# Performance work log

Measured on AMD Instinct MI355X. Metric: run time of the kernel, lower is better.

Reference implementation:

```python
import jax, jax.numpy as jnp
import numpy as np

EPS = 1e-6
NH, HD = 8, 16            # num_heads, head_dim (dim=128)
KSS, DILS, HPR = (3, 5), (1, 2), (6, 2)  # kernel sizes, dilations, heads per range (favor_small)


def gelu(t):
    return jax.nn.gelu(t, approximate=False)


def conv1x1(x, w, b):
    # x: (B,C,H,W), w: (O,C), b: (O,)
    return jnp.einsum('oc,bchw->bohw', w, x) + b[None, :, None, None]


def dwconv(x, w, b, dil=1):
    # depthwise conv, w: (C,1,k,k)
    k = w.shape[-1]
    p = (k // 2) * dil
    y = jax.lax.conv_general_dilated(
        x, w, window_strides=(1, 1), padding=[(p, p), (p, p)],
        rhs_dilation=(dil, dil), feature_group_count=x.shape[1],
        dimension_numbers=('NCHW', 'OIHW', 'NCHW'))
    return y + b[None, :, None, None]


def ln2d(x, w, b):
    # LayerNorm over channel dim of NCHW
    mu = x.mean(axis=1, keepdims=True)
    var = ((x - mu) ** 2).mean(axis=1, keepdims=True)
    return (x - mu) * jax.lax.rsqrt(var + EPS) * w[None, :, None, None] + b[None, :, None, None]


def unfold(x, ks, dil):
    # x: (B,h,d,H,W) -> (B,h,d,L,H,W) with L=ks*ks neighborhood (row-major, matches F.unfold)
    B, h, d, H, W = x.shape
    p = (ks // 2) * dil
    xp = jnp.pad(x, ((0, 0), (0, 0), (0, 0), (p, p), (p, p)))
    patches = [xp[..., i * dil:i * dil + H, j * dil:j * dil + W]
               for i in range(ks) for j in range(ks)]
    return jnp.stack(patches, axis=3)


def neighborhood_attn(x, qkv_ws, qkv_bs, proj_w, proj_b):
    B, C, H, W = x.shape
    scale = HD ** -0.5
    outs, hs = [], 0
    for i in range(2):
        qkv = conv1x1(x, qkv_ws[i], qkv_bs[i]).reshape(B, 3, NH, HD, H, W)
        he = hs + HPR[i]
        q, k, v = qkv[:, 0, hs:he], qkv[:, 1, hs:he], qkv[:, 2, hs:he]
        k_nb = unfold(k, KSS[i], DILS[i])  # (B,h,d,L,H,W)
        v_nb = unfold(v, KSS[i], DILS[i])
        logits = jnp.einsum('bhdxy,bhdlxy->bhlxy', q * scale, k_nb)
        attn = jax.nn.softmax(logits, axis=2)
        outs.append(jnp.einsum('bhlxy,bhdlxy->bhdxy', attn, v_nb))
        hs = he
    out = jnp.concatenate(outs, axis=1).reshape(B, C, H, W)
    return conv1x1(out, proj_w, proj_b)


def msconvstar(x, fc1_w, fc1_b, dw_ws, dw_bs, fc2_w, fc2_b):
    h = conv1x1(x, fc1_w, fc1_b)                  # (B,192,H,W)
    xs = jnp.split(h, [64, 128], axis=1)          # channels [64,64,64] for dw_sizes (1,3,5)
    ys = [dwconv(t, w, b) for t, w, b in zip(xs, dw_ws, dw_bs)]
    h = h + jnp.concatenate(ys, axis=1)
    x1, x2 = jnp.split(h, 2, axis=1)
    return conv1x1(gelu(x1) * x2, fc2_w, fc2_b)


def cascaded_sparse(x, dw0_w, dw0_b, dw1_w, dw1_b, pw_w, pw_b):
    x = gelu(dwconv(x, dw0_w, dw0_b, dil=1))
    x = gelu(dwconv(x, dw1_w, dw1_b, dil=2))
    return conv1x1(x, pw_w, pw_b)


def setup_inputs() -> dict:
    key = jax.random.key(0)
    ks = jax.random.split(key, 24)
    C, HID = 128, 192

    def p(k, shape, s=0.02):
        return jax.random.normal(k, shape, jnp.float32) * s

    d = {'x': jax.random.normal(ks[0], (4, C, 80, 80), jnp.float32)}
    for i in (1, 2, 3, 4):
        d[f'n{i}_w'] = jnp.ones((C,), jnp.float32)
        d[f'n{i}_b'] = jnp.zeros((C,), jnp.float32)
    d['qkv0_w'] = p(ks[1], (3 * C, C)); d['qkv0_b'] = jnp.zeros((3 * C,), jnp.float32)
    d['qkv1_w'] = p(ks[2], (3 * C, C)); d['qkv1_b'] = jnp.zeros((3 * C,), jnp.float32)
    d['ma_proj_w'] = p(ks[3], (C, C)); d['ma_proj_b'] = jnp.zeros((C,), jnp.float32)
    for pre, k0 in (('m1', 4), ('m2', 10)):
        d[f'{pre}_fc1_w'] = p(ks[k0], (HID, C)); d[f'{pre}_fc1_b'] = jnp.zeros((HID,), jnp.float32)
        for j, dk in enumerate((1, 3, 5)):
            d[f'{pre}_dw{j}_w'] = p(ks[k0 + 1 + j], (64, 1, dk, dk))
            d[f'{pre}_dw{j}_b'] = jnp.zeros((64,), jnp.float32)
        d[f'{pre}_fc2_w'] = p(ks[k0 + 4], (C, HID // 2)); d[f'{pre}_fc2_b'] = jnp.zeros((C,), jnp.float32)
    d['sma_dw0_w'] = p(ks[16], (C, 1, 3, 3)); d['sma_dw0_b'] = jnp.zeros((C,), jnp.float32)
    d['sma_dw1_w'] = p(ks[17], (C, 1, 3, 3)); d['sma_dw1_b'] = jnp.zeros((C,), jnp.float32)
    d['sma_pw_w'] = p(ks[18], (C, C)); d['sma_pw_b'] = jnp.zeros((C,), jnp.float32)
    return d


def reference(x, n1_w, n1_b, n2_w, n2_b, n3_w, n3_b, n4_w, n4_b,
              qkv0_w, qkv0_b, qkv1_w, qkv1_b, ma_proj_w, ma_proj_b,
              m1_fc1_w, m1_fc1_b, m1_dw0_w, m1_dw0_b, m1_dw1_w, m1_dw1_b,
              m1_dw2_w, m1_dw2_b, m1_fc2_w, m1_fc2_b,
              sma_dw0_w, sma_dw0_b, sma_dw1_w, sma_dw1_b, sma_pw_w, sma_pw_b,
              m2_fc1_w, m2_fc1_b, m2_dw0_w, m2_dw0_b, m2_dw1_w, m2_dw1_b,
              m2_dw2_w, m2_dw2_b, m2_fc2_w, m2_fc2_b):
    x = x + neighborhood_attn(ln2d(x, n1_w, n1_b), (qkv0_w, qkv1_w), (qkv0_b, qkv1_b), ma_proj_w, ma_proj_b)
    x = x + msconvstar(ln2d(x, n2_w, n2_b), m1_fc1_w, m1_fc1_b,
                       (m1_dw0_w, m1_dw1_w, m1_dw2_w), (m1_dw0_b, m1_dw1_b, m1_dw2_b), m1_fc2_w, m1_fc2_b)
    x = x + cascaded_sparse(ln2d(x, n3_w, n3_b), sma_dw0_w, sma_dw0_b, sma_dw1_w, sma_dw1_b, sma_pw_w, sma_pw_b)
    x = x + msconvstar(ln2d(x, n4_w, n4_b), m2_fc1_w, m2_fc1_b,
                       (m2_dw0_w, m2_dw1_w, m2_dw2_w), (m2_dw0_b, m2_dw1_b, m2_dw2_b), m2_fc2_w, m2_fc2_b)
    return x
```

## Files before the change

### kernel.cpp

```cpp
#include <hip/hip_runtime.h>
#include <math.h>

#define Hn 80
#define Wn 80
#define HWn 6400

typedef unsigned short u16;
typedef __attribute__((ext_vector_type(8))) short s16x8;
typedef __attribute__((ext_vector_type(4))) float f32x4;

__device__ __forceinline__ float gelu_exact(float v) {
  return 0.5f * v * (1.f + erff(v * 0.70710678118654752f));
}
__device__ __forceinline__ u16 f2bf(float x) {
  unsigned u = __float_as_uint(x);
  return (u16)((u + 0x7fffu + ((u >> 16) & 1u)) >> 16);
}
__device__ __forceinline__ float bf2f(u16 h) {
  return __uint_as_float(((unsigned)h) << 16);
}
typedef __attribute__((address_space(1))) const unsigned int* gptr_t;
typedef __attribute__((address_space(3))) unsigned int* lptr_t;
__device__ __forceinline__ void gld16(const void* g, void* l) {
  __builtin_amdgcn_global_load_lds((gptr_t)g, (lptr_t)l, 16, 0, 0);
}
__device__ __forceinline__ void ld16h(const u16* p, float* f) {
  uint4 a = *(const uint4*)p;
  uint4 c = *(const uint4*)(p + 8);
  unsigned w[8] = {a.x, a.y, a.z, a.w, c.x, c.y, c.z, c.w};
  #pragma unroll
  for (int j = 0; j < 8; ++j) {
    f[2 * j]     = __uint_as_float(w[j] << 16);
    f[2 * j + 1] = __uint_as_float(w[j] & 0xffff0000u);
  }
}

__global__ __launch_bounds__(256) void wprep_k(
    const float* __restrict__ q0w, const float* __restrict__ q0b,
    const float* __restrict__ q1w, const float* __restrict__ q1b,
    const float* __restrict__ projw, const float* __restrict__ f1w_1,
    const float* __restrict__ f2w_1, const float* __restrict__ pww,
    const float* __restrict__ f1w_2, const float* __restrict__ f2w_2,
    u16* Wq, float* Bq, u16* Wp, u16* Wf1a, u16* Wf2a, u16* Wpw, u16* Wf1b, u16* Wf2b) {
  int idx = blockIdx.x * 256 + threadIdx.x;
  if (idx < 49152) {
    int r = idx >> 7, ic = idx & 127;
    int sel = r >> 7, c = r & 127;
    const float* src = ((c >> 4) < 6 ? q0w : q1w);
    Wq[idx] = f2bf(src[(size_t)(sel * 128 + c) * 128 + ic]);
    return;
  }
  idx -= 49152;
  if (idx < 16384) { Wp[idx] = f2bf(projw[idx]); return; }
  idx -= 16384;
  if (idx < 24576) { Wf1a[idx] = f2bf(f1w_1[idx]); return; }
  idx -= 24576;
  if (idx < 16384) { int oc = idx >> 7, ic = idx & 127;
    Wf2a[idx] = ic < 96 ? f2bf(f2w_1[oc * 96 + ic]) : (u16)0; return; }
  idx -= 16384;
  if (idx < 16384) { Wpw[idx] = f2bf(pww[idx]); return; }
  idx -= 16384;
  if (idx < 24576) { Wf1b[idx] = f2bf(f1w_2[idx]); return; }
  idx -= 24576;
  if (idx < 16384) { int oc = idx >> 7, ic = idx & 127;
    Wf2b[idx] = ic < 96 ? f2bf(f2w_2[oc * 96 + ic]) : (u16)0; return; }
  idx -= 16384;
  if (idx < 384) {
    int sel = idx >> 7, c = idx & 127;
    Bq[idx] = ((c >> 4) < 6 ? q0b : q1b)[sel * 128 + c];
  }
}

__global__ __launch_bounds__(256) void ln_k(const float* __restrict__ in,
    const float* __restrict__ gw, const float* __restrict__ gb, u16* __restrict__ outv) {
  __shared__ float sS[4][64];
  __shared__ float sQ[4][64];
  __shared__ unsigned sT[64 * 64];
  const int b = blockIdx.y;
  const int p0 = blockIdx.x * 64;
  const int tid = threadIdx.x;
  const int px = tid & 63;
  const int cg = tid >> 6;
  const float* ip = in + (size_t)b * 128 * HWn + p0 + px;
  float s = 0.f, q = 0.f;
  #pragma unroll 8
  for (int c = cg * 32; c < cg * 32 + 32; ++c) { float v = ip[(size_t)c * HWn]; s += v; q += v * v; }
  sS[cg][px] = s; sQ[cg][px] = q;
  __syncthreads();
  float S = sS[0][px] + sS[1][px] + sS[2][px] + sS[3][px];
  float Q = sQ[0][px] + sQ[1][px] + sQ[2][px] + sQ[3][px];
  float mu = S * (1.f / 128.f);
  float rs = rsqrtf(Q * (1.f / 128.f) - mu * mu + 1e-6f);
  #pragma unroll
  for (int j = 0; j < 16; ++j) {
    int c0 = cg * 32 + 2 * j;
    float v0 = ip[(size_t)c0 * HWn];
    float v1 = ip[(size_t)(c0 + 1) * HWn];
    v0 = (v0 - mu) * rs * gw[c0] + gb[c0];
    v1 = (v1 - mu) * rs * gw[c0 + 1] + gb[c0 + 1];
    int wc = cg * 16 + j;
    sT[px * 64 + (wc ^ (px & 31))] = (unsigned)f2bf(v0) | ((unsigned)f2bf(v1) << 16);
  }
  __syncthreads();
  u16* ob = outv + ((size_t)b * HWn + p0) * 128;
  #pragma unroll
  for (int it = 0; it < 4; ++it) {
    int opx = it * 16 + (tid >> 4);
    int chunk = tid & 15;
    unsigned w[4];
    #pragma unroll
    for (int j = 0; j < 4; ++j)
      w[j] = sT[opx * 64 + ((chunk * 4 + j) ^ (opx & 31))];
    *(uint4*)(ob + (size_t)opx * 128 + chunk * 8) = make_uint4(w[0], w[1], w[2], w[3]);
  }
}

__device__ __forceinline__ s16x8 ldfrag(const u16* s, int row, int gk) {
  return *(const s16x8*)(s + row * 128 + ((gk ^ (row & 7)) << 3));
}

template<int ORIENT, int SPLITQ, int H16>
__global__ __launch_bounds__(256) void gemm_k(
    const u16* __restrict__ Xg, const u16* __restrict__ Wg,
    const float* __restrict__ bias, u16* __restrict__ outH, int OCT) {
  __shared__ u16 sX[128 * 128];
  __shared__ u16 sW[64 * 128];
  const int tid = threadIdx.x, lane = tid & 63, wv = tid >> 6;
  const int b = blockIdx.y;
  const int px0 = blockIdx.x * 128;
  const int oc0 = blockIdx.z * 64;
  const u16* xb = Xg + ((size_t)b * HWn + px0) * 128;
  const u16* wb = Wg + (size_t)oc0 * 128;
  #pragma unroll
  for (int i = 0; i < 8; ++i) {
    int o16 = (wv * 8 + i) * 64 + lane;
    int r = o16 >> 4, g = o16 & 15;
    gld16(xb + (size_t)r * 128 + ((g ^ (r & 7)) << 3), (char*)sX + (size_t)(wv * 8 + i) * 1024);
  }
  #pragma unroll
  for (int i = 0; i < 4; ++i) {
    int o16 = (wv * 4 + i) * 64 + lane;
    int r = o16 >> 4, g = o16 & 15;
    gld16(wb + (size_t)r * 128 + ((g ^ (r & 7)) << 3), (char*)sW + (size_t)(wv * 4 + i) * 1024);
  }
  __syncthreads();
  const int l15 = lane & 15, l4 = lane >> 4;
  if (ORIENT == 0) {
    f32x4 acc[4][2] = {};
    #pragma unroll
    for (int ks = 0; ks < 4; ++ks) {
      int gk = ks * 4 + l4;
      s16x8 a[4], bb[2];
      #pragma unroll
      for (int mi = 0; mi < 4; ++mi) a[mi] = ldfrag(sW, mi * 16 + l15, gk);
      #pragma unroll
      for (int ni = 0; ni < 2; ++ni) bb[ni] = ldfrag(sX, wv * 32 + ni * 16 + l15, gk);
      #pragma unroll
      for (int mi = 0; mi < 4; ++mi)
        #pragma unroll
        for (int ni = 0; ni < 2; ++ni)
          acc[mi][ni] = __builtin_amdgcn_mfma_f32_16x16x32_bf16(a[mi], bb[ni], acc[mi][ni], 0, 0, 0);
    }
    #pragma unroll
    for (int mi = 0; mi < 4; ++mi) {
      #pragma unroll
      for (int rr = 0; rr < 4; ++rr) {
        int oc = oc0 + mi * 16 + l4 * 4 + rr;
        float bv = bias[oc];
        #pragma unroll
        for (int ni = 0; ni < 2; ++ni) {
          size_t idx = ((size_t)b * OCT + oc) * HWn + px0 + wv * 32 + ni * 16 + l15;
          outH[idx] = f2bf(acc[mi][ni][rr] + bv);
        }
      }
    }
  } else {
    f32x4 acc[2][4] = {};
    #pragma unroll
    for (int ks = 0; ks < 4; ++ks) {
      int gk = ks * 4 + l4;
      s16x8 a[2], bb[4];
      #pragma unroll
      for (int mi = 0; mi < 2; ++mi) a[mi] = ldfrag(sX, wv * 32 + mi * 16 + l15, gk);
      #pragma unroll
      for (int ni = 0; ni < 4; ++ni) bb[ni] = ldfrag(sW, ni * 16 + l15, gk);
      #pragma unroll
      for (int mi = 0; mi < 2; ++mi)
        #pragma unroll
        for (int ni = 0; ni < 4; ++ni)
          acc[mi][ni] = __builtin_amdgcn_mfma_f32_16x16x32_bf16(a[mi], bb[ni], acc[mi][ni], 0, 0, 0);
    }
    #pragma unroll
    for (int ni = 0; ni < 4; ++ni) {
      int oc = oc0 + ni * 16 + l15;
      float bv = bias[oc];
      #pragma unroll
      for (int mi = 0; mi < 2; ++mi) {
        #pragma unroll
        for (int rr = 0; rr < 4; ++rr) {
          int px = px0 + wv * 32 + mi * 16 + l4 * 4 + rr;
          float v = acc[mi][ni][rr] + bv;
          u16 hv = f2bf(v);
          int sel = oc >> 7, c = oc & 127;
          int head = c >> 4, d = c & 15;
          outH[((((size_t)sel * 8 + head) * 4 + b) * HWn + px) * 16 + d] = hv;
        }
      }
    }
  }
}

template<int EPI>
__global__ __launch_bounds__(256) void gemm64_k(
    const u16* __restrict__ Xg, const u16* __restrict__ Wg,
    const float* __restrict__ bias, const float* __restrict__ resid,
    float* __restrict__ outF, u16* __restrict__ outLN, float2* __restrict__ stats,
    const float* __restrict__ gw, const float* __restrict__ gb) {
  __shared__ u16 sX[64 * 128];
  __shared__ u16 sW[128 * 128];
  const int tid = threadIdx.x, lane = tid & 63, wv = tid >> 6;
  const int b = blockIdx.y;
  const int px0 = blockIdx.x * 64;
  const u16* xb = Xg + ((size_t)b * HWn + px0) * 128;
  #pragma unroll
  for (int i = 0; i < 4; ++i) {
    int o16 = (wv * 4 + i) * 64 + lane;
    int r = o16 >> 4, g = o16 & 15;
    gld16(xb + (size_t)r * 128 + ((g ^ (r & 7)) << 3), (char*)sX + (size_t)(wv * 4 + i) * 1024);
  }
  #pragma unroll
  for (int i = 0; i < 8; ++i) {
    int o16 = (wv * 8 + i) * 64 + lane;
    int r = o16 >> 4, g = o16 & 15;
    gld16(Wg + (size_t)r * 128 + ((g ^ (r & 7)) << 3), (char*)sW + (size_t)(wv * 8 + i) * 1024);
  }
  __syncthreads();
  const int l15 = lane & 15, l4 = lane >> 4;
  f32x4 acc[8] = {};
  #pragma unroll
  for (int ks = 0; ks < 4; ++ks) {
    int gk = ks * 4 + l4;
    s16x8 bb = ldfrag(sX, wv * 16 + l15, gk);
    #pragma unroll
    for (int mi = 0; mi < 8; ++mi) {
      s16x8 a = ldfrag(sW, mi * 16 + l15, gk);
      acc[mi] = __builtin_amdgcn_mfma_f32_16x16x32_bf16(a, bb, acc[mi], 0, 0, 0);
    }
  }
  const int pxg = px0 + wv * 16 + l15;
  float v[8][4];
  float s = 0.f, q = 0.f;
  #pragma unroll
  for (int mi = 0; mi < 8; ++mi) {
    #pragma unroll
    for (int rr = 0; rr < 4; ++rr) {
      int oc = mi * 16 + l4 * 4 + rr;
      float t = acc[mi][rr] + bias[oc];
      t += resid[((size_t)b * 128 + oc) * HWn + pxg];
      v[mi][rr] = t;
      s += t;
      q = fmaf(t, t, q);
    }
  }
  #pragma unroll
  for (int mi = 0; mi < 8; ++mi)
    #pragma unroll
    for (int rr = 0; rr < 4; ++rr) {
      int oc = mi * 16 + l4 * 4 + rr;
      outF[((size_t)b * 128 + oc) * HWn + pxg] = v[mi][rr];
    }
  if (EPI == 0) return;
  s += __shfl_xor(s, 16); s += __shfl_xor(s, 32);
  q += __shfl_xor(q, 16); q += __shfl_xor(q, 32);
  float mu = s * (1.f / 128.f);
  float rs = rsqrtf(q * (1.f / 128.f) - mu * mu + 1e-6f);
  if (EPI == 1) {
    u16* lp = outLN + ((size_t)b * HWn + pxg) * 128;
    #pragma unroll
    for (int mi = 0; mi < 8; ++mi) {
      int oc0 = mi * 16 + l4 * 4;
      unsigned lo = (unsigned)f2bf((v[mi][0] - mu) * rs * gw[oc0] + gb[oc0])
                  | ((unsigned)f2bf((v[mi][1] - mu) * rs * gw[oc0 + 1] + gb[oc0 + 1]) << 16);
      unsigned hi = (unsigned)f2bf((v[mi][2] - mu) * rs * gw[oc0 + 2] + gb[oc0 + 2])
                  | ((unsigned)f2bf((v[mi][3] - mu) * rs * gw[oc0 + 3] + gb[oc0 + 3]) << 16);
      *(uint2*)(lp + oc0) = make_uint2(lo, hi);
    }
  } else {
    if (l4 == 0) stats[(size_t)b * HWn + pxg] = make_float2(mu, rs);
  }
}

template<int KS, int DIL>
__device__ __forceinline__ void natt_body(const u16* __restrict__ qkv,
    u16* __restrict__ out, u16* __restrict__ sK, u16* __restrict__ sV,
    int b, int h, int ty0, int tx0, int tid, int ly, int lx) {
  constexpr int HALO = DIL * (KS / 2);
  constexpr int D = 16 + 2 * HALO;
  const u16* Qb = qkv + (((size_t)h * 4 + b) * HWn) * 16;
  const u16* Kb = qkv + ((((size_t)8 + h) * 4 + b) * HWn) * 16;
  const u16* Vb = qkv + ((((size_t)16 + h) * 4 + b) * HWn) * 16;
  for (int i = tid; i < D * D * 2; i += 256) {
    int pxi = i >> 1, half = i & 1;
    int ey = pxi / D, ex = pxi - ey * D;
    int gy = ty0 - HALO + ey, gx = tx0 - HALO + ex;
    uint4 kv = make_uint4(0, 0, 0, 0), vv = make_uint4(0, 0, 0, 0);
    if (gy >= 0 && gy < Hn && gx >= 0 && gx < Wn) {
      size_t off = (size_t)(gy * Wn + gx) * 16 + half * 8;
      kv = *(const uint4*)(Kb + off);
      vv = *(const uint4*)(Vb + off);
    }
    *(uint4*)(sK + pxi * 16 + half * 8) = kv;
    *(uint4*)(sV + pxi * 16 + half * 8) = vv;
  }
  const int p = (ty0 + ly) * Wn + tx0 + lx;
  float qv[16];
  ld16h(Qb + (size_t)p * 16, qv);
  #pragma unroll
  for (int d = 0; d < 16; ++d) qv[d] *= 0.25f;
  __syncthreads();
  constexpr int L = KS * KS;
  float lg[L];
  #pragma unroll
  for (int i = 0; i < KS; ++i) {
    #pragma unroll
    for (int j = 0; j < KS; ++j) {
      float kvv[16];
      ld16h(sK + (size_t)((ly + i * DIL) * D + lx + j * DIL) * 16, kvv);
      float a = 0.f;
      #pragma unroll
      for (int d = 0; d < 16; ++d) a = fmaf(qv[d], kvv[d], a);
      lg[i * KS + j] = a;
    }
  }
  float mx = lg[0];
  #pragma unroll
  for (int l = 1; l < L; ++l) mx = fmaxf(mx, lg[l]);
  float sum = 0.f;
  #pragma unroll
  for (int l = 0; l < L; ++l) { float e = __expf(lg[l] - mx); lg[l] = e; sum += e; }
  float inv = 1.f / sum;
  float acc[16];
  #pragma unroll
  for (int d = 0; d < 16; ++d) acc[d] = 0.f;
  #pragma unroll
  for (int i = 0; i < KS; ++i) {
    #pragma unroll
    for (int j = 0; j < KS; ++j) {
      float vv[16];
      ld16h(sV + (size_t)((ly + i * DIL) * D + lx + j * DIL) * 16, vv);
      float wl = lg[i * KS + j] * inv;
      #pragma unroll
      for (int d = 0; d < 16; ++d) acc[d] = fmaf(wl, vv[d], acc[d]);
    }
  }
  unsigned wst[8];
  #pragma unroll
  for (int j = 0; j < 8; ++j)
    wst[j] = (unsigned)f2bf(acc[2 * j]) | ((unsigned)f2bf(acc[2 * j + 1]) << 16);
  u16* op = out + ((size_t)b * HWn + p) * 128 + h * 16;
  *(uint4*)op = make_uint4(wst[0], wst[1], wst[2], wst[3]);
  *(uint4*)(op + 8) = make_uint4(wst[4], wst[5], wst[6], wst[7]);
}

__global__ __launch_bounds__(256) void natt_k(const u16* __restrict__ qkv,
                                              u16* __restrict__ out) {
  __shared__ u16 sK[24 * 24 * 16];
  __shared__ u16 sV[24 * 24 * 16];
  const int b = blockIdx.y, h = blockIdx.z;
  const int tile = blockIdx.x;
  const int ty0 = (tile / 5) * 16, tx0 = (tile % 5) * 16;
  const int tid = threadIdx.x;
  const int ly = tid >> 4, lx = tid & 15;
  if (h < 6) natt_body<3, 1>(qkv, out, sK, sV, b, h, ty0, tx0, tid, ly, lx);
  else       natt_body<5, 2>(qkv, out, sK, sV, b, h, ty0, tx0, tid, ly, lx);
}

template<int R>
__device__ __forceinline__ void stage_plane(const u16* __restrict__ plane,
                                            float* __restrict__ s,
                                            int ty0, int tx0, int tid) {
  constexpr int D = 16 + 2 * R, PD = D + 1;
  #pragma unroll
  for (int i = tid; i < D * D; i += 256) {
    int ey = i / D, ex = i - ey * D;
    int gy = ty0 - R + ey, gx = tx0 - R + ex;
    float v = 0.f;
    if (gy >= 0 && gy < Hn && gx >= 0 && gx < Wn) v = bf2f(plane[gy * Wn + gx]);
    s[ey * PD + ex] = v;
  }
}

template<int R>
__device__ __forceinline__ float dw_from_lds(const float* __restrict__ s, int ly, int lx,
                                             const float* __restrict__ w, float bv) {
  constexpr int PD = 16 + 2 * R + 1;
  float center = s[(ly + R) * PD + (lx + R)];
  float acc = bv;
  #pragma unroll
  for (int i = 0; i < 2 * R + 1; ++i)
    #pragma unroll
    for (int j = 0; j < 2 * R + 1; ++j)
      acc = fmaf(w[i * (2 * R + 1) + j], s[(ly + i) * PD + (lx + j)], acc);
  return center + acc;
}

template<int R1, int R2>
__device__ __forceinline__ void star_pairs(const u16* __restrict__ hb,
    const float* __restrict__ w0, const float* __restrict__ b0,
    const float* __restrict__ w1, const float* __restrict__ b1,
    const float* __restrict__ w2, const float* __restrict__ b2,
    float* __restrict__ s1_0, float* __restrict__ s1_1,
    float* __restrict__ s2_0, float* __restrict__ s2_1,
    int z, int ty0, int tx0, int tid, int ly, int lx, unsigned* __restrict__ res) {
  if (R1 > 0) stage_plane<R1>(hb + (size_t)(z * 8) * HWn, s1_0, ty0, tx0, tid);
  stage_plane<R2>(hb + (size_t)(z * 8 + 96) * HWn, s2_0, ty0, tx0, tid);
  __syncthreads();
  #pragma unroll 1
  for (int pi = 0; pi < 8; ++pi) {
    int c1 = z * 8 + pi;
    int c2 = c1 + 96;
    float* s1c = (pi & 1) ? s1_1 : s1_0;
    float* s2c = (pi & 1) ? s2_1 : s2_0;
    if (pi < 7) {
      float* s1n = (pi & 1) ? s1_0 : s1_1;
      float* s2n = (pi & 1) ? s2_0 : s2_1;
      if (R1 > 0) stage_plane<R1>(hb + (size_t)(c1 + 1) * HWn, s1n, ty0, tx0, tid);
      stage_plane<R2>(hb + (size_t)(c2 + 1) * HWn, s2n, ty0, tx0, tid);
    }
    float h1;
    if constexpr (R1 == 0) {
      float cen = bf2f(hb[(size_t)c1 * HWn + (ty0 + ly) * Wn + tx0 + lx]);
      h1 = cen + fmaf(cen, w0[c1], b0[c1]);
    } else {
      h1 = dw_from_lds<R1>(s1c, ly, lx, w1 + (c1 - 64) * 9, b1[c1 - 64]);
    }
    float h2;
    if constexpr (R2 == 1) {
      h2 = dw_from_lds<1>(s2c, ly, lx, w1 + (c2 - 64) * 9, b1[c2 - 64]);
    } else {
      h2 = dw_from_lds<2>(s2c, ly, lx, w2 + (c2 - 128) * 25, b2[c2 - 128]);
    }
    u16 gv = f2bf(gelu_exact(h1) * h2);
    if (pi & 1) res[pi >> 1] |= ((unsigned)gv) << 16;
    else        res[pi >> 1] = (unsigned)gv;
    __syncthreads();
  }
}

__global__ __launch_bounds__(256) void star_k(const u16* __restrict__ hbuf,
    const float* __restrict__ w0, const float* __restrict__ b0,
    const float* __restrict__ w1, const float* __restrict__ b1,
    const float* __restrict__ w2, const float* __restrict__ b2,
    u16* __restrict__ g) {
  __shared__ float s1_0[18 * 19];
  __shared__ float s1_1[18 * 19];
  __shared__ float s2_0[20 * 21];
  __shared__ float s2_1[20 * 21];
  const int b = blockIdx.y, z = blockIdx.z;
  const int tile = blockIdx.x;
  const int ty0 = (tile / 5) * 16, tx0 = (tile % 5) * 16;
  const int tid = threadIdx.x;
  const int ly = tid >> 4, lx = tid & 15;
  const u16* hb = hbuf + (size_t)b * 192 * HWn;
  unsigned res[4];
  if (z < 4)      star_pairs<0, 1>(hb, w0, b0, w1, b1, w2, b2, s1_0, s1_1, s2_0, s2_1, z, ty0, tx0, tid, ly, lx, res);
  else if (z < 8) star_pairs<0, 2>(hb, w0, b0, w1, b1, w2, b2, s1_0, s1_1, s2_0, s2_1, z, ty0, tx0, tid, ly, lx, res);
  else            star_pairs<1, 2>(hb, w0, b0, w1, b1, w2, b2, s1_0, s1_1, s2_0, s2_1, z, ty0, tx0, tid, ly, lx, res);
  const int px = (ty0 + ly) * Wn + tx0 + lx;
  *(uint4*)(g + ((size_t)b * HWn + px) * 128 + z * 8) = make_uint4(res[0], res[1], res[2], res[3]);
  if (z < 4)
    *(uint4*)(g + ((size_t)b * HWn + px) * 128 + 96 + z * 8) = make_uint4(0, 0, 0, 0);
}

__global__ __launch_bounds__(256) void dwgf_k(const float* __restrict__ xin,
    const float2* __restrict__ st,
    const float* __restrict__ gw, const float* __restrict__ gb,
    const float* __restrict__ w1, const float* __restrict__ b1,
    const float* __restrict__ w2, const float* __restrict__ b2,
    u16* __restrict__ out) {
  __shared__ float sA[22 * 23];
  __shared__ float sB[20 * 21];
  __shared__ float sMu[22 * 22];
  __shared__ float sRs[22 * 22];
  const int b = blockIdx.y, z = blockIdx.z;
  const int tile = blockIdx.x;
  const int ty0 = (tile / 5) * 16, tx0 = (tile % 5) * 16;
  const int tid = threadIdx.x;
  const int ly = tid >> 4, lx = tid & 15;
  #pragma unroll
  for (int i = tid; i < 22 * 22; i += 256) {
    int ey = i / 22, ex = i - ey * 22;
    int gy = ty0 - 3 + ey, gx = tx0 - 3 + ex;
    float2 s = make_float2(0.f, 0.f);
    if (gy >= 0 && gy < Hn && gx >= 0 && gx < Wn) s = st[(size_t)b * HWn + gy * Wn + gx];
    sMu[i] = s.x; sRs[i] = s.y;
  }
  const float* xb = xin + (size_t)b * 128 * HWn;
  unsigned res[4];
  #pragma unroll 1
  for (int ci = 0; ci < 8; ++ci) {
    int c = z * 8 + ci;
    const float* xp = xb + (size_t)c * HWn;
    float gwc = gw[c], gbc = gb[c];
    __syncthreads();
    #pragma unroll
    for (int i = tid; i < 22 * 22; i += 256) {
      int ey = i / 22, ex = i - ey * 22;
      int gy = ty0 - 3 + ey, gx = tx0 - 3 + ex;
      float v = 0.f;
      if (gy >= 0 && gy < Hn && gx >= 0 && gx < Wn)
        v = (xp[gy * Wn + gx] - sMu[i]) * sRs[i] * gwc + gbc;
      sA[ey * 23 + ex] = v;
    }
    __syncthreads();
    #pragma unroll
    for (int j = tid; j < 20 * 20; j += 256) {
      int by = j / 20, bx = j - by * 20;
      int gy = ty0 - 2 + by, gx = tx0 - 2 + bx;
      float r = 0.f;
      if (gy >= 0 && gy < Hn && gx >= 0 && gx < Wn) {
        float acc = b1[c];
        #pragma unroll
        for (int di = 0; di < 3; ++di)
          #pragma unroll
          for (int dj = 0; dj < 3; ++dj)
            acc = fmaf(w1[c * 9 + di * 3 + dj], sA[(by + di) * 23 + (bx + dj)], acc);
        r = gelu_exact(acc);
      }
      sB[by * 21 + bx] = r;
    }
    __syncthreads();
    float acc = b2[c];
    #pragma unroll
    for (int di = 0; di < 3; ++di)
      #pragma unroll
      for (int dj = 0; dj < 3; ++dj)
        acc = fmaf(w2[c * 9 + di * 3 + dj], sB[(ly + 2 * di) * 21 + (lx + 2 * dj)], acc);
    float r = gelu_exact(acc);
    u16 gv = f2bf(r);
    if (ci & 1) res[ci >> 1] |= ((unsigned)gv) << 16;
    else        res[ci >> 1] = (unsigned)gv;
  }
  const int px = (ty0 + ly) * Wn + tx0 + lx;
  *(uint4*)(out + ((size_t)b * HWn + px) * 128 + z * 8) = make_uint4(res[0], res[1], res[2], res[3]);
}

extern "C" void kernel_launch(void* const* d_in, const int* in_sizes, int n_in,
                              void* d_out, int out_size, void* d_ws, size_t ws_size,
                              hipStream_t stream) {
  (void)in_sizes; (void)n_in; (void)out_size; (void)ws_size;
  const float* x      = (const float*)d_in[0];
  const float* n1w    = (const float*)d_in[1];
  const float* n1b    = (const float*)d_in[2];
  const float* n2w    = (const float*)d_in[3];
  const float* n2b    = (const float*)d_in[4];
  const float* n3w    = (const float*)d_in[5];
  const float* n3b    = (const float*)d_in[6];
  const float* n4w    = (const float*)d_in[7];
  const float* n4b    = (const float*)d_in[8];
  const float* qkv0w  = (const float*)d_in[9];
  const float* qkv0b  = (const float*)d_in[10];
  const float* qkv1w  = (const float*)d_in[11];
  const float* qkv1b  = (const float*)d_in[12];
  const float* projw  = (const float*)d_in[13];
  const float* projb  = (const float*)d_in[14];
  const float* m1fc1w = (const float*)d_in[15];
  const float* m1fc1b = (const float*)d_in[16];
  const float* m1dw0w = (const float*)d_in[17];
  const float* m1dw0b = (const float*)d_in[18];
  const float* m1dw1w = (const float*)d_in[19];
  const float* m1dw1b = (const float*)d_in[20];
  const float* m1dw2w = (const float*)d_in[21];
  const float* m1dw2b = (const float*)d_in[22];
  const float* m1fc2w = (const float*)d_in[23];
  const float* m1fc2b = (const float*)d_in[24];
  const float* smadw0w = (const float*)d_in[25];
  const float* smadw0b = (const float*)d_in[26];
  const float* smadw1w = (const float*)d_in[27];
  const float* smadw1b = (const float*)d_in[28];
  const float* smapww  = (const float*)d_in[29];
  const float* smapwb  = (const float*)d_in[30];
  const float* m2fc1w = (const float*)d_in[31];
  const float* m2fc1b = (const float*)d_in[32];
  const float* m2dw0w = (const float*)d_in[33];
  const float* m2dw0b = (const float*)d_in[34];
  const float* m2dw1w = (const float*)d_in[35];
  const float* m2dw1b = (const float*)d_in[36];
  const float* m2dw2w = (const float*)d_in[37];
  const float* m2dw2b = (const float*)d_in[38];
  const float* m2fc2w = (const float*)d_in[39];
  const float* m2fc2b = (const float*)d_in[40];

  float* out = (float*)d_out;
  char* wsb = (char*)d_ws;
  u16*  QKV = (u16*)(wsb + 0);
  u16*  Hb16 = (u16*)(wsb + 0);
  u16*  LNo = (u16*)(wsb + 19660800);
  u16*  ATT = (u16*)(wsb + 26214400);
  u16*  T2  = (u16*)(wsb + 32768000);
  char* wp = wsb + 39321600;
  u16* Wq    = (u16*)wp;  wp += 98304;
  u16* Wproj = (u16*)wp;  wp += 32768;
  u16* Wf1a  = (u16*)wp;  wp += 49152;
  u16* Wf2a  = (u16*)wp;  wp += 32768;
  u16* Wpw   = (u16*)wp;  wp += 32768;
  u16* Wf1b  = (u16*)wp;  wp += 49152;
  u16* Wf2b  = (u16*)wp;  wp += 32768;
  float* Bq  = (float*)wp; wp += 2048;
  float2* Stats = (float2*)wp;

  dim3 blk(256);
  wprep_k<<<642, blk, 0, stream>>>(qkv0w, qkv0b, qkv1w, qkv1b, projw, m1fc1w, m1fc2w,
                                   smapww, m2fc1w, m2fc2w,
                                   Wq, Bq, Wproj, Wf1a, Wf2a, Wpw, Wf1b, Wf2b);

  ln_k<<<dim3(100, 4), blk, 0, stream>>>(x, n1w, n1b, LNo);
  gemm_k<1, 1, 0><<<dim3(50, 4, 6), blk, 0, stream>>>(LNo, Wq, Bq, QKV, 384);
  natt_k<<<dim3(25, 4, 8), blk, 0, stream>>>(QKV, ATT);
  gemm64_k<1><<<dim3(100, 4), blk, 0, stream>>>(ATT, Wproj, projb, x, out, LNo, nullptr, n2w, n2b);

  gemm_k<0, 0, 1><<<dim3(50, 4, 3), blk, 0, stream>>>(LNo, Wf1a, m1fc1b, Hb16, 192);
  star_k<<<dim3(25, 4, 12), blk, 0, stream>>>(Hb16, m1dw0w, m1dw0b, m1dw1w, m1dw1b, m1dw2w, m1dw2b, ATT);
  gemm64_k<2><<<dim3(100, 4), blk, 0, stream>>>(ATT, Wf2a, m1fc2b, out, out, nullptr, Stats, nullptr, nullptr);

  dwgf_k<<<dim3(25, 4, 16), blk, 0, stream>>>(out, Stats, n3w, n3b,
                                              smadw0w, smadw0b, smadw1w, smadw1b, T2);
  gemm64_k<1><<<dim3(100, 4), blk, 0, stream>>>(T2, Wpw, smapwb, out, out, LNo, nullptr, n4w, n4b);

  gemm_k<0, 0, 1><<<dim3(50, 4, 3), blk, 0, stream>>>(LNo, Wf1b, m2fc1b, Hb16, 192);
  star_k<<<dim3(25, 4, 12), blk, 0, stream>>>(Hb16, m2dw0w, m2dw0b, m2dw1w, m2dw1b, m2dw2w, m2dw2b, ATT);
  gemm64_k<0><<<dim3(100, 4), blk, 0, stream>>>(ATT, Wf2b, m2fc2b, out, out, nullptr, nullptr, nullptr, nullptr);
}
```

Before: 166.3 us.

## Halve gemm64 pixel tile with cross-wave LN reduction; use polynomial erf in GELU

```diff
diff --git a/kernel.cpp b/kernel.cpp
--- a/kernel.cpp
+++ b/kernel.cpp
@@ -10,7 +10,13 @@
 typedef __attribute__((ext_vector_type(4))) float f32x4;
 
 __device__ __forceinline__ float gelu_exact(float v) {
-  return 0.5f * v * (1.f + erff(v * 0.70710678118654752f));
+  float x = fabsf(v) * 0.70710678118654752f;
+  float t = 1.f / (1.f + 0.3275911f * x);
+  float p = t * (0.254829592f + t * (-0.284496736f + t * (1.421413741f +
+            t * (-1.453152027f + t * 1.061405429f))));
+  float erfa = 1.f - p * __expf(-x * x);
+  float erfv = copysignf(erfa, v);
+  return 0.5f * v * (1.f + erfv);
 }
 __device__ __forceinline__ u16 f2bf(float x) {
   unsigned u = __float_as_uint(x);
@@ -216,69 +222,73 @@
     const float* __restrict__ bias, const float* __restrict__ resid,
     float* __restrict__ outF, u16* __restrict__ outLN, float2* __restrict__ stats,
     const float* __restrict__ gw, const float* __restrict__ gb) {
-  __shared__ u16 sX[64 * 128];
+  __shared__ u16 sX[32 * 128];
   __shared__ u16 sW[128 * 128];
   const int tid = threadIdx.x, lane = tid & 63, wv = tid >> 6;
   const int b = blockIdx.y;
-  const int px0 = blockIdx.x * 64;
+  const int px0 = blockIdx.x * 32;
   const u16* xb = Xg + ((size_t)b * HWn + px0) * 128;
   #pragma unroll
-  for (int i = 0; i < 4; ++i) {
-    int o16 = (wv * 4 + i) * 64 + lane;
+  for (int i = 0; i < 2; ++i) {
+    int o16 = i * 256 + tid;
     int r = o16 >> 4, g = o16 & 15;
-    gld16(xb + (size_t)r * 128 + ((g ^ (r & 7)) << 3), (char*)sX + (size_t)(wv * 4 + i) * 1024);
+    gld16(xb + (size_t)r * 128 + ((g ^ (r & 7)) << 3), (char*)sX + (size_t)o16 * 16);
   }
   #pragma unroll
   for (int i = 0; i < 8; ++i) {
-    int o16 = (wv * 8 + i) * 64 + lane;
+    int o16 = i * 256 + tid;
     int r = o16 >> 4, g = o16 & 15;
-    gld16(Wg + (size_t)r * 128 + ((g ^ (r & 7)) << 3), (char*)sW + (size_t)(wv * 8 + i) * 1024);
+    gld16(Wg + (size_t)r * 128 + ((g ^ (r & 7)) << 3), (char*)sW + (size_t)o16 * 16);
   }
   __syncthreads();
   const int l15 = lane & 15, l4 = lane >> 4;
-  f32x4 acc[8] = {};
+  const int h = wv >> 1, oh = wv & 1;
+  f32x4 acc[4] = {};
   #pragma unroll
   for (int ks = 0; ks < 4; ++ks) {
     int gk = ks * 4 + l4;
-    s16x8 bb = ldfrag(sX, wv * 16 + l15, gk);
-    #pragma unroll
-    for (int mi = 0; mi < 8; ++mi) {
-      s16x8 a = ldfrag(sW, mi * 16 + l15, gk);
+    s16x8 bb = ldfrag(sX, h * 16 + l15, gk);
+    #pragma unroll
+    for (int mi = 0; mi < 4; ++mi) {
+      s16x8 a = ldfrag(sW, oh * 64 + mi * 16 + l15, gk);
       acc[mi] = __builtin_amdgcn_mfma_f32_16x16x32_bf16(a, bb, acc[mi], 0, 0, 0);
     }
   }
-  const int pxg = px0 + wv * 16 + l15;
-  float v[8][4];
+  const int pxg = px0 + h * 16 + l15;
+  float v[4][4];
   float s = 0.f, q = 0.f;
   #pragma unroll
-  for (int mi = 0; mi < 8; ++mi) {
+  for (int mi = 0; mi < 4; ++mi) {
     #pragma unroll
     for (int rr = 0; rr < 4; ++rr) {
-      int oc = mi * 16 + l4 * 4 + rr;
+      int oc = oh * 64 + mi * 16 + l4 * 4 + rr;
       float t = acc[mi][rr] + bias[oc];
       t += resid[((size_t)b * 128 + oc) * HWn + pxg];
       v[mi][rr] = t;
       s += t;
       q = fmaf(t, t, q);
-    }
-  }
-  #pragma unroll
-  for (int mi = 0; mi < 8; ++mi)
-    #pragma unroll
-    for (int rr = 0; rr < 4; ++rr) {
-      int oc = mi * 16 + l4 * 4 + rr;
-      outF[((size_t)b * 128 + oc) * HWn + pxg] = v[mi][rr];
-    }
+      outF[((size_t)b * 128 + oc) * HWn + pxg] = t;
+    }
+  }
   if (EPI == 0) return;
   s += __shfl_xor(s, 16); s += __shfl_xor(s, 32);
   q += __shfl_xor(q, 16); q += __shfl_xor(q, 32);
-  float mu = s * (1.f / 128.f);
-  float rs = rsqrtf(q * (1.f / 128.f) - mu * mu + 1e-6f);
+  float* sRed = (float*)sX;
+  __syncthreads();
+  if (lane < 16) {
+    sRed[(h * 2 + oh) * 16 + l15] = s;
+    sRed[64 + (h * 2 + oh) * 16 + l15] = q;
+  }
+  __syncthreads();
+  float S = sRed[(h * 2) * 16 + l15] + sRed[(h * 2 + 1) * 16 + l15];
+  float Q = sRed[64 + (h * 2) * 16 + l15] + sRed[64 + (h * 2 + 1) * 16 + l15];
+  float mu = S * (1.f / 128.f);
+  float rs = rsqrtf(Q * (1.f / 128.f) - mu * mu + 1e-6f);
   if (EPI == 1) {
     u16* lp = outLN + ((size_t)b * HWn + pxg) * 128;
     #pragma unroll
-    for (int mi = 0; mi < 8; ++mi) {
-      int oc0 = mi * 16 + l4 * 4;
+    for (int mi = 0; mi < 4; ++mi) {
+      int oc0 = oh * 64 + mi * 16 + l4 * 4;
       unsigned lo = (unsigned)f2bf((v[mi][0] - mu) * rs * gw[oc0] + gb[oc0])
                   | ((unsigned)f2bf((v[mi][1] - mu) * rs * gw[oc0 + 1] + gb[oc0 + 1]) << 16);
       unsigned hi = (unsigned)f2bf((v[mi][2] - mu) * rs * gw[oc0 + 2] + gb[oc0 + 2])
@@ -286,7 +296,7 @@
       *(uint2*)(lp + oc0) = make_uint2(lo, hi);
     }
   } else {
-    if (l4 == 0) stats[(size_t)b * HWn + pxg] = make_float2(mu, rs);
+    if (oh == 0 && lane < 16) stats[(size_t)b * HWn + pxg] = make_float2(mu, rs);
   }
 }
 
@@ -617,17 +627,17 @@
   ln_k<<<dim3(100, 4), blk, 0, stream>>>(x, n1w, n1b, LNo);
   gemm_k<1, 1, 0><<<dim3(50, 4, 6), blk, 0, stream>>>(LNo, Wq, Bq, QKV, 384);
   natt_k<<<dim3(25, 4, 8), blk, 0, stream>>>(QKV, ATT);
-  gemm64_k<1><<<dim3(100, 4), blk, 0, stream>>>(ATT, Wproj, projb, x, out, LNo, nullptr, n2w, n2b);
+  gemm64_k<1><<<dim3(200, 4), blk, 0, stream>>>(ATT, Wproj, projb, x, out, LNo, nullptr, n2w, n2b);
 
   gemm_k<0, 0, 1><<<dim3(50, 4, 3), blk, 0, stream>>>(LNo, Wf1a, m1fc1b, Hb16, 192);
   star_k<<<dim3(25, 4, 12), blk, 0, stream>>>(Hb16, m1dw0w, m1dw0b, m1dw1w, m1dw1b, m1dw2w, m1dw2b, ATT);
-  gemm64_k<2><<<dim3(100, 4), blk, 0, stream>>>(ATT, Wf2a, m1fc2b, out, out, nullptr, Stats, nullptr, nullptr);
+  gemm64_k<2><<<dim3(200, 4), blk, 0, stream>>>(ATT, Wf2a, m1fc2b, out, out, nullptr, Stats, nullptr, nullptr);
 
   dwgf_k<<<dim3(25, 4, 16), blk, 0, stream>>>(out, Stats, n3w, n3b,
                                               smadw0w, smadw0b, smadw1w, smadw1b, T2);
-  gemm64_k<1><<<dim3(100, 4), blk, 0, stream>>>(T2, Wpw, smapwb, out, out, LNo, nullptr, n4w, n4b);
+  gemm64_k<1><<<dim3(200, 4), blk, 0, stream>>>(T2, Wpw, smapwb, out, out, LNo, nullptr, n4w, n4b);
 
   gemm_k<0, 0, 1><<<dim3(50, 4, 3), blk, 0, stream>>>(LNo, Wf1b, m2fc1b, Hb16, 192);
   star_k<<<dim3(25, 4, 12), blk, 0, stream>>>(Hb16, m2dw0w, m2dw0b, m2dw1w, m2dw1b, m2dw2w, m2dw2b, ATT);
-  gemm64_k<0><<<dim3(100, 4), blk, 0, stream>>>(ATT, Wf2b, m2fc2b, out, out, nullptr, nullptr, nullptr, nullptr);
-}
+  gemm64_k<0><<<dim3(200, 4), blk, 0, stream>>>(ATT, Wf2b, m2fc2b, out, out, nullptr, nullptr, nullptr, nullptr);
+}
```

After: 157.2 us. 5.4% less time.
